# Performance work log

Hardware: AMD Instinct MI355X
Metric: run time of the kernel (lower is better)

The kernel has to match this reference:

```python
import jax, jax.numpy as jnp
import numpy as np

BATCH, SEQ, IN_DIM, HID = 256, 256, 128, 512
KMAX, MID, NCLS = 4, 256, 16  # maxout features, maxout/dense/highway width, output classes


def hard_sigmoid(x):
    return jnp.clip(0.2 * x + 0.5, 0.0, 1.0)


def setup_inputs() -> dict:
    key = jax.random.key(0)
    ks = jax.random.split(key, 20)
    s = 0.05
    d = {
        'x': jax.random.normal(ks[0], (BATCH, SEQ, IN_DIM), jnp.float32),
        'W_z': jax.random.normal(ks[1], (IN_DIM, HID), jnp.float32) * s,
        'W_r': jax.random.normal(ks[2], (IN_DIM, HID), jnp.float32) * s,
        'W_h': jax.random.normal(ks[3], (IN_DIM, HID), jnp.float32) * s,
        'U_z': jax.random.normal(ks[4], (HID, HID), jnp.float32) * s,
        'U_r': jax.random.normal(ks[5], (HID, HID), jnp.float32) * s,
        'U_h': jax.random.normal(ks[6], (HID, HID), jnp.float32) * s,
        'b_z': jax.random.normal(ks[7], (HID,), jnp.float32) * s,
        'b_r': jax.random.normal(ks[8], (HID,), jnp.float32) * s,
        'b_h': jax.random.normal(ks[9], (HID,), jnp.float32) * s,
        'mo_W': jax.random.normal(ks[10], (KMAX, HID, MID), jnp.float32) * s,
        'mo_b': jax.random.normal(ks[11], (KMAX, MID), jnp.float32) * s,
        'd1_W': jax.random.normal(ks[12], (MID, MID), jnp.float32) * s,
        'd1_b': jax.random.normal(ks[13], (MID,), jnp.float32) * s,
        'hw_W': jax.random.normal(ks[14], (MID, MID), jnp.float32) * s,
        'hw_b': jax.random.normal(ks[15], (MID,), jnp.float32) * s,
        'hw_Wc': jax.random.normal(ks[16], (MID, MID), jnp.float32) * s,
        'hw_bc': jax.random.normal(ks[17], (MID,), jnp.float32) * s,
        'd2_W': jax.random.normal(ks[18], (MID, NCLS), jnp.float32) * s,
        'd2_b': jax.random.normal(ks[19], (NCLS,), jnp.float32) * s,
    }
    return d


def reference(x, W_z, W_r, W_h, U_z, U_r, U_h, b_z, b_r, b_h,
              mo_W, mo_b, d1_W, d1_b, hw_W, hw_b, hw_Wc, hw_bc, d2_W, d2_b):
    # ---- Theano-convention GRU (reset applied before U_h matmul) ----
    # Precompute all input projections in one batched GEMM each: [B,S,H]
    xz = jnp.einsum('bsi,ih->bsh', x, W_z) + b_z
    xr = jnp.einsum('bsi,ih->bsh', x, W_r) + b_r
    xh = jnp.einsum('bsi,ih->bsh', x, W_h) + b_h

    def step(h, xs):
        xzt, xrt, xht = xs
        z = hard_sigmoid(xzt + h @ U_z)
        r = hard_sigmoid(xrt + h @ U_r)
        hh = jnp.tanh(xht + (r * h) @ U_h)
        h_new = z * h + (1.0 - z) * hh
        return h_new, None

    h0 = jnp.zeros((x.shape[0], U_z.shape[0]), x.dtype)
    # scan over time axis: move S to leading dim
    xs = (jnp.swapaxes(xz, 0, 1), jnp.swapaxes(xr, 0, 1), jnp.swapaxes(xh, 0, 1))
    h, _ = jax.lax.scan(step, h0, xs)

    # ---- Maxout dense ----
    h = jnp.max(jnp.einsum('bi,kio->bko', h, mo_W) + mo_b, axis=1)
    # ---- Dense (linear) ----
    h = h @ d1_W + d1_b
    # ---- Highway ----
    t = jax.nn.sigmoid(h @ hw_Wc + hw_bc)
    hh = jax.nn.relu(h @ hw_W + hw_b)
    h = t * hh + (1.0 - t) * h
    # ---- Dense + softmax ----
    logits = h @ d2_W + d2_b
    return jax.nn.softmax(logits, axis=-1)
```

## Files before the change

### kernel.cpp

```cpp
#include <hip/hip_runtime.h>
#include <hip/hip_bf16.h>
#include <math.h>

#define BATCH 256
#define SEQN  256
#define INDIM 128
#define HID   512
#define MID   256
#define NCLS  16

#define NG 8
#define RG 32
#define NS 16
#define SC 32

typedef _Float16 half8 __attribute__((ext_vector_type(8)));
typedef float    f32x4 __attribute__((ext_vector_type(4)));

__device__ __forceinline__ half8 cc_load16(const _Float16* p) {
    half8 r;
    asm volatile("global_load_dwordx4 %0, %1, off sc1" : "=&v"(r) : "v"(p));
    return r;
}
__device__ __forceinline__ void cc_wait() {
    asm volatile("s_waitcnt vmcnt(0)" ::: "memory");
    __builtin_amdgcn_sched_barrier(0);
}
__device__ __forceinline__ void cc_store16(_Float16* p, _Float16 v) {
    unsigned short u = __builtin_bit_cast(unsigned short, v);
    asm volatile("global_store_short %0, %1, off sc1" :: "v"(p), "v"(u) : "memory");
}
__device__ __forceinline__ void cc_store_u32(unsigned int* p, unsigned int v) {
    asm volatile("global_store_dword %0, %1, off sc1" :: "v"(p), "v"(v) : "memory");
}
__device__ __forceinline__ unsigned int cc_load_u32(const unsigned int* p) {
    unsigned int r;
    asm volatile("global_load_dword %0, %1, off sc1\n\ts_waitcnt vmcnt(0)"
                 : "=&v"(r) : "v"(p) : "memory");
    return r;
}

__device__ __forceinline__ void wait_flags(const unsigned int* base, int s,
                                           int l, unsigned int tgt) {
    const int slot = l & 15;
    for (;;) {
        unsigned int v = cc_load_u32(base + slot);
        int ok = (slot == s) || (v >= tgt);
        if (__all(ok)) break;
    }
}

__global__ __launch_bounds__(256) void pack_wA(
    const float* __restrict__ Uz, const float* __restrict__ Ur,
    const float* __restrict__ Wz, const float* __restrict__ Wr,
    _Float16* __restrict__ out)
{
    int idx = blockIdx.x * 256 + threadIdx.x;
    int j = idx & 7, l = (idx >> 3) & 63;
    int fr = idx >> 9;
    int kt = fr % 20; int r2 = fr / 20;
    int nt4 = r2 & 3; int s = r2 >> 2;
    int k = kt * 32 + (l >> 4) * 8 + j;
    int col = s * SC + (nt4 & 1) * 16 + (l & 15);
    const float* U = (nt4 < 2) ? Uz : Ur;
    const float* W = (nt4 < 2) ? Wz : Wr;
    float v = (k < HID) ? U[k * HID + col] : W[(k - HID) * HID + col];
    out[idx] = (_Float16)v;
}

__global__ __launch_bounds__(256) void pack_wB(
    const float* __restrict__ Uh, const float* __restrict__ Wh,
    _Float16* __restrict__ out)
{
    int idx = blockIdx.x * 256 + threadIdx.x;
    int j = idx & 7, l = (idx >> 3) & 63;
    int fr = idx >> 9;
    int kt = fr % 20; int r2 = fr / 20;
    int nt2 = r2 & 1; int s = r2 >> 1;
    int k = kt * 32 + (l >> 4) * 8 + j;
    int col = s * SC + nt2 * 16 + (l & 15);
    float v = (k < HID) ? Uh[k * HID + col] : Wh[(k - HID) * HID + col];
    out[idx] = (_Float16)v;
}

__global__ __launch_bounds__(512) void gru_sync(
    const float* __restrict__ x, const _Float16* __restrict__ GWA,
    const _Float16* __restrict__ GWB,
    const float* __restrict__ bz, const float* __restrict__ br,
    const float* __restrict__ bh,
    _Float16* __restrict__ HF, _Float16* __restrict__ VF,
    unsigned int* __restrict__ arr, float* __restrict__ hout)
{
    __shared__ __attribute__((aligned(16))) _Float16 WA[4][20][64][8];
    __shared__ __attribute__((aligned(16))) _Float16 WB[2][20][64][8];
    __shared__ float HO[RG][SC];

    const int tid = threadIdx.x;
    const int w = tid >> 6, l = tid & 63;
    const int bid = blockIdx.x;
    const int g = bid & 7, s = bid >> 3;
    const int m = l & 15;
    const int crow0 = (l >> 4) * 4;

    const int mt  = w & 1;
    const int nt4 = w >> 1;
    const int nt2 = w >> 1;

    {
        const float4* srcA = (const float4*)&GWA[(size_t)s * (4 * 20 * 512)];
        float4* dstA = (float4*)&WA[0][0][0][0];
        for (int i = tid; i < 4 * 20 * 512 / 8; i += 512) dstA[i] = srcA[i];
        const float4* srcB = (const float4*)&GWB[(size_t)s * (2 * 20 * 512)];
        float4* dstB = (float4*)&WB[0][0][0][0];
        for (int i = tid; i < 2 * 20 * 512 / 8; i += 512) dstB[i] = srcB[i];
    }
    for (int i = tid; i < RG * SC; i += 512) ((float*)HO)[i] = 0.f;

    float biasA;
    {
        int col = s * SC + (nt4 & 1) * 16 + m;
        biasA = (nt4 < 2) ? bz[col] : br[col];
    }
    float biasB = 0.f;
    if (w < 4) biasB = bh[s * SC + nt2 * 16 + m];

    unsigned int* f1base = &arr[g * 16];
    unsigned int* f2base = &arr[128 + g * 16];
    unsigned int* f1own  = &arr[g * 16 + s];
    unsigned int* f2own  = &arr[128 + g * 16 + s];
    __syncthreads();

    float zreg[4];
    half8 xfr[4];

    for (int t = 0; t < SEQN; ++t) {
        float4 xa[4], xb[4];
        {
            const float* xp = &x[(((size_t)(g * RG + mt * 16 + m)) * SEQN + t) * INDIM + (l >> 4) * 8];
            #pragma unroll
            for (int kf = 0; kf < 4; ++kf) {
                xa[kf] = *(const float4*)(xp + kf * 32);
                xb[kf] = *(const float4*)(xp + kf * 32 + 4);
            }
        }

        wait_flags(f2base, s, l, (unsigned int)t);

        half8 hfr[16];
        {
            const _Float16* hf = &HF[(size_t)(g * 2 + mt) * 16 * 512];
            #pragma unroll
            for (int kt = 0; kt < 16; ++kt)
                hfr[kt] = cc_load16(hf + kt * 512 + l * 8);
        }
        #pragma unroll
        for (int kf = 0; kf < 4; ++kf) {
            half8 hx;
            hx[0] = (_Float16)xa[kf].x; hx[1] = (_Float16)xa[kf].y;
            hx[2] = (_Float16)xa[kf].z; hx[3] = (_Float16)xa[kf].w;
            hx[4] = (_Float16)xb[kf].x; hx[5] = (_Float16)xb[kf].y;
            hx[6] = (_Float16)xb[kf].z; hx[7] = (_Float16)xb[kf].w;
            xfr[kf] = hx;
        }
        cc_wait();

        {
            f32x4 acc = {0.f, 0.f, 0.f, 0.f};
            #pragma unroll
            for (int kt = 0; kt < 16; ++kt) {
                half8 bf = *(const half8*)&WA[nt4][kt][l][0];
                acc = __builtin_amdgcn_mfma_f32_16x16x32_f16(hfr[kt], bf, acc, 0, 0, 0);
            }
            #pragma unroll
            for (int kf = 0; kf < 4; ++kf) {
                half8 bf = *(const half8*)&WA[nt4][16 + kf][l][0];
                acc = __builtin_amdgcn_mfma_f32_16x16x32_f16(xfr[kf], bf, acc, 0, 0, 0);
            }
            if (nt4 < 2) {
                #pragma unroll
                for (int ri = 0; ri < 4; ++ri) {
                    float pre = acc[ri] + biasA;
                    zreg[ri] = fminf(fmaxf(0.2f * pre + 0.5f, 0.f), 1.f);
                }
            } else {
                #pragma unroll
                for (int ri = 0; ri < 4; ++ri) {
                    float pre = acc[ri] + biasA;
                    float gr = fminf(fmaxf(0.2f * pre + 0.5f, 0.f), 1.f);
                    int rloc = mt * 16 + crow0 + ri;
                    int cs = (nt4 & 1) * 16 + m;
                    float vv = gr * HO[rloc][cs];
                    cc_store16(&VF[(((size_t)(g * 2 + mt) * 16 + s) * 64 +
                                    ((crow0 + ri) + 16 * (cs >> 3))) * 8 + (cs & 7)],
                               (_Float16)vv);
                }
            }
        }

        asm volatile("s_waitcnt vmcnt(0)" ::: "memory");
        __syncthreads();
        if (tid == 0) cc_store_u32(f1own, (unsigned int)(t + 1));

        if (w < 4) {
            wait_flags(f1base, s, l, (unsigned int)(t + 1));

            half8 vfr[16];
            {
                const _Float16* vf = &VF[(size_t)(g * 2 + mt) * 16 * 512];
                #pragma unroll
                for (int kt = 0; kt < 16; ++kt)
                    vfr[kt] = cc_load16(vf + kt * 512 + l * 8);
            }
            cc_wait();

            f32x4 acc2 = {0.f, 0.f, 0.f, 0.f};
            #pragma unroll
            for (int kt = 0; kt < 16; ++kt) {
                half8 bf = *(const half8*)&WB[nt2][kt][l][0];
                acc2 = __builtin_amdgcn_mfma_f32_16x16x32_f16(vfr[kt], bf, acc2, 0, 0, 0);
            }
            #pragma unroll
            for (int kf = 0; kf < 4; ++kf) {
                half8 bf = *(const half8*)&WB[nt2][16 + kf][l][0];
                acc2 = __builtin_amdgcn_mfma_f32_16x16x32_f16(xfr[kf], bf, acc2, 0, 0, 0);
            }
            #pragma unroll
            for (int ri = 0; ri < 4; ++ri) {
                float pre = acc2[ri] + biasB;
                float e  = __expf(2.f * pre);
                float hh = 1.f - 2.f / (e + 1.f);
                int rloc = mt * 16 + crow0 + ri;
                int cs = nt2 * 16 + m;
                float zz = zreg[ri];
                float ho = HO[rloc][cs];
                float hn = zz * ho + (1.f - zz) * hh;
                HO[rloc][cs] = hn;
                cc_store16(&HF[(((size_t)(g * 2 + mt) * 16 + s) * 64 +
                                ((crow0 + ri) + 16 * (cs >> 3))) * 8 + (cs & 7)],
                           (_Float16)hn);
            }
        }

        asm volatile("s_waitcnt vmcnt(0)" ::: "memory");
        __syncthreads();
        if (tid == 0) cc_store_u32(f2own, (unsigned int)(t + 1));
    }

    for (int i = tid; i < RG * SC; i += 512) {
        int r = i >> 5, c = i & 31;
        hout[(size_t)(g * RG + r) * HID + s * SC + c] = HO[r][c];
    }
}

__global__ __launch_bounds__(256) void maxout_k(
    const float* __restrict__ h, const float* __restrict__ moW,
    const float* __restrict__ mob, float* __restrict__ m)
{
    const int ot = blockIdx.x, bt = blockIdx.y;
    __shared__ float sA[32][33];
    __shared__ float sB[4][32][33];
    const int tid = threadIdx.x;
    const int tx = tid & 15, ty = tid >> 4;
    const int b0 = bt * 32, o0 = ot * 32;
    const int lr = tid >> 3, lk4 = (tid & 7) << 2;

    float acc[4][2][2];
    #pragma unroll
    for (int p = 0; p < 4; ++p)
        acc[p][0][0] = acc[p][0][1] = acc[p][1][0] = acc[p][1][1] = 0.f;

    for (int kt = 0; kt < 16; ++kt) {
        const int k0 = kt * 32;
        float4 a = *reinterpret_cast<const float4*>(&h[(b0 + lr) * HID + k0 + lk4]);
        float4 wv[4];
        #pragma unroll
        for (int p = 0; p < 4; ++p)
            wv[p] = *reinterpret_cast<const float4*>(&moW[((size_t)p * HID + k0 + lr) * MID + o0 + lk4]);
        __syncthreads();
        sA[lk4+0][lr] = a.x; sA[lk4+1][lr] = a.y; sA[lk4+2][lr] = a.z; sA[lk4+3][lr] = a.w;
        #pragma unroll
        for (int p = 0; p < 4; ++p) {
            sB[p][lr][lk4+0] = wv[p].x; sB[p][lr][lk4+1] = wv[p].y;
            sB[p][lr][lk4+2] = wv[p].z; sB[p][lr][lk4+3] = wv[p].w;
        }
        __syncthreads();
        #pragma unroll
        for (int kk = 0; kk < 32; ++kk) {
            float a0 = sA[kk][ty*2], a1 = sA[kk][ty*2+1];
            #pragma unroll
            for (int p = 0; p < 4; ++p) {
                float w0 = sB[p][kk][tx*2], w1 = sB[p][kk][tx*2+1];
                acc[p][0][0] += a0*w0; acc[p][0][1] += a0*w1;
                acc[p][1][0] += a1*w0; acc[p][1][1] += a1*w1;
            }
        }
    }

    #pragma unroll
    for (int q = 0; q < 2; ++q)
        #pragma unroll
        for (int c = 0; c < 2; ++c) {
            const int row = b0 + ty*2 + q, col = o0 + tx*2 + c;
            float best = -1e30f;
            #pragma unroll
            for (int p = 0; p < 4; ++p)
                best = fmaxf(best, acc[p][q][c] + mob[p * MID + col]);
            m[row * MID + col] = best;
        }
}

__global__ __launch_bounds__(256) void dense1_k(
    const float* __restrict__ m, const float* __restrict__ W,
    const float* __restrict__ b, float* __restrict__ a1)
{
    const int jt = blockIdx.x, bt = blockIdx.y;
    __shared__ float sA[32][33];
    __shared__ float sB[32][33];
    const int tid = threadIdx.x;
    const int tx = tid & 15, ty = tid >> 4;
    const int b0 = bt * 32, j0 = jt * 32;
    const int lr = tid >> 3, lk4 = (tid & 7) << 2;

    float acc[2][2] = {{0.f,0.f},{0.f,0.f}};

    for (int kt = 0; kt < 8; ++kt) {
        const int k0 = kt * 32;
        float4 a  = *reinterpret_cast<const float4*>(&m[(b0 + lr) * MID + k0 + lk4]);
        float4 bv = *reinterpret_cast<const float4*>(&W[(k0 + lr) * MID + j0 + lk4]);
        __syncthreads();
        sA[lk4+0][lr] = a.x; sA[lk4+1][lr] = a.y; sA[lk4+2][lr] = a.z; sA[lk4+3][lr] = a.w;
        sB[lr][lk4+0] = bv.x; sB[lr][lk4+1] = bv.y; sB[lr][lk4+2] = bv.z; sB[lr][lk4+3] = bv.w;
        __syncthreads();
        #pragma unroll
        for (int kk = 0; kk < 32; ++kk) {
            float a0 = sA[kk][ty*2], a1v = sA[kk][ty*2+1];
            float w0 = sB[kk][tx*2], w1 = sB[kk][tx*2+1];
            acc[0][0] += a0*w0; acc[0][1] += a0*w1;
            acc[1][0] += a1v*w0; acc[1][1] += a1v*w1;
        }
    }

    #pragma unroll
    for (int q = 0; q < 2; ++q)
        #pragma unroll
        for (int c = 0; c < 2; ++c) {
            const int row = b0 + ty*2 + q, col = j0 + tx*2 + c;
            a1[row * MID + col] = acc[q][c] + b[col];
        }
}

__global__ __launch_bounds__(256) void highway_k(
    const float* __restrict__ a1,
    const float* __restrict__ hwW, const float* __restrict__ hwb,
    const float* __restrict__ hwWc, const float* __restrict__ hwbc,
    float* __restrict__ h2)
{
    const int jt = blockIdx.x, bt = blockIdx.y;
    __shared__ float sA[32][33];
    __shared__ float sBh[32][33];
    __shared__ float sBc[32][33];
    const int tid = threadIdx.x;
    const int tx = tid & 15, ty = tid >> 4;
    const int b0 = bt * 32, j0 = jt * 32;
    const int lr = tid >> 3, lk4 = (tid & 7) << 2;

    float acch[2][2] = {{0.f,0.f},{0.f,0.f}};
    float accc[2][2] = {{0.f,0.f},{0.f,0.f}};

    for (int kt = 0; kt < 8; ++kt) {
        const int k0 = kt * 32;
        float4 a   = *reinterpret_cast<const float4*>(&a1[(b0 + lr) * MID + k0 + lk4]);
        float4 bh4 = *reinterpret_cast<const float4*>(&hwW[(k0 + lr) * MID + j0 + lk4]);
        float4 bc4 = *reinterpret_cast<const float4*>(&hwWc[(k0 + lr) * MID + j0 + lk4]);
        __syncthreads();
        sA[lk4+0][lr] = a.x; sA[lk4+1][lr] = a.y; sA[lk4+2][lr] = a.z; sA[lk4+3][lr] = a.w;
        sBh[lr][lk4+0] = bh4.x; sBh[lr][lk4+1] = bh4.y; sBh[lr][lk4+2] = bh4.z; sBh[lr][lk4+3] = bh4.w;
        sBc[lr][lk4+0] = bc4.x; sBc[lr][lk4+1] = bc4.y; sBc[lr][lk4+2] = bc4.z; sBc[lr][lk4+3] = bc4.w;
        __syncthreads();
        #pragma unroll
        for (int kk = 0; kk < 32; ++kk) {
            float a0 = sA[kk][ty*2], a1v = sA[kk][ty*2+1];
            float h0 = sBh[kk][tx*2], h1 = sBh[kk][tx*2+1];
            float c0 = sBc[kk][tx*2], c1 = sBc[kk][tx*2+1];
            acch[0][0] += a0*h0; acch[0][1] += a0*h1;
            acch[1][0] += a1v*h0; acch[1][1] += a1v*h1;
            accc[0][0] += a0*c0; accc[0][1] += a0*c1;
            accc[1][0] += a1v*c0; accc[1][1] += a1v*c1;
        }
    }

    #pragma unroll
    for (int q = 0; q < 2; ++q)
        #pragma unroll
        for (int c = 0; c < 2; ++c) {
            const int row = b0 + ty*2 + q, col = j0 + tx*2 + c;
            float tt = 1.f / (1.f + expf(-(accc[q][c] + hwbc[col])));
            float hp = fmaxf(acch[q][c] + hwb[col], 0.f);
            float av = a1[row * MID + col];
            h2[row * MID + col] = tt * hp + (1.f - tt) * av;
        }
}

__global__ __launch_bounds__(256) void d2_softmax(
    const float* __restrict__ h2, const float* __restrict__ W,
    const float* __restrict__ b, float* __restrict__ out)
{
    const int b0 = blockIdx.x * 16;
    const int r = threadIdx.x >> 4, c = threadIdx.x & 15;
    const int row = b0 + r;

    float acc = b[c];
    for (int i = 0; i < MID; ++i)
        acc += h2[row * MID + i] * W[i * NCLS + c];

    float mx = acc;
    #pragma unroll
    for (int off = 8; off; off >>= 1)
        mx = fmaxf(mx, __shfl_xor(mx, off, 16));
    float e = expf(acc - mx);
    float sm = e;
    #pragma unroll
    for (int off = 8; off; off >>= 1)
        sm += __shfl_xor(sm, off, 16);
    out[row * NCLS + c] = e / sm;
}

extern "C" void kernel_launch(void* const* d_in, const int* in_sizes, int n_in,
                              void* d_out, int out_size, void* d_ws, size_t ws_size,
                              hipStream_t stream) {
    (void)in_sizes; (void)n_in; (void)out_size; (void)ws_size;

    const float* x    = (const float*)d_in[0];
    const float* Wz   = (const float*)d_in[1];
    const float* Wr   = (const float*)d_in[2];
    const float* Wh   = (const float*)d_in[3];
    const float* Uz   = (const float*)d_in[4];
    const float* Ur   = (const float*)d_in[5];
    const float* Uh   = (const float*)d_in[6];
    const float* bz   = (const float*)d_in[7];
    const float* br   = (const float*)d_in[8];
    const float* bh   = (const float*)d_in[9];
    const float* moW  = (const float*)d_in[10];
    const float* mob  = (const float*)d_in[11];
    const float* d1W  = (const float*)d_in[12];
    const float* d1b  = (const float*)d_in[13];
    const float* hwW  = (const float*)d_in[14];
    const float* hwb  = (const float*)d_in[15];
    const float* hwWc = (const float*)d_in[16];
    const float* hwbc = (const float*)d_in[17];
    const float* d2W  = (const float*)d_in[18];
    const float* d2b  = (const float*)d_in[19];
    float* out = (float*)d_out;

    char* ws = (char*)d_ws;
    _Float16* GWA = (_Float16*)(ws + 0);
    _Float16* GWB = (_Float16*)(ws + 1310720);
    _Float16* HF  = (_Float16*)(ws + 1966080);
    _Float16* VF  = (_Float16*)(ws + 2228224);
    unsigned int* arr = (unsigned int*)(ws + 2490368);
    float*    hbuf = (float*)(ws + 2494464);
    float*    mxb = (float*)(ws + 0);
    float*    a1b = (float*)(ws + 262144);
    float*    h2b = (float*)(ws + 524288);

    hipMemsetAsync(HF, 0, 262144, stream);
    hipMemsetAsync(arr, 0, 4096, stream);

    pack_wA<<<2560, 256, 0, stream>>>(Uz, Ur, Wz, Wr, GWA);
    pack_wB<<<1280, 256, 0, stream>>>(Uh, Wh, GWB);

    gru_sync<<<128, 512, 0, stream>>>(x, GWA, GWB, bz, br, bh, HF, VF, arr, hbuf);

    dim3 blk(256);
    maxout_k<<<dim3(8, 8), blk, 0, stream>>>(hbuf, moW, mob, mxb);
    dense1_k<<<dim3(8, 8), blk, 0, stream>>>(mxb, d1W, d1b, a1b);
    highway_k<<<dim3(8, 8), blk, 0, stream>>>(a1b, hwW, hwb, hwWc, hwbc, h2b);
    d2_softmax<<<16, blk, 0, stream>>>(h2b, d2W, d2b, out);
}
```

Before: 1.742 ms.

## Replace block-wide barriers with per-wave flag handshakes and double-buffer hidden state

Splits the GRU block's waves into r-gate producers and z/candidate consumers that synchronize through per-wave global flags instead of __syncthreads plus one block flag. The shared hidden-state buffer is double-buffered by timestep parity, so the next step's writes do not race with readers of the current step. The aim is to cut the barrier and serialization latency on the recurrent critical path. In exchange there are many more flag slots to poll, with finer-grained spinning and a larger workspace layout.

```diff
diff --git a/kernel.cpp b/kernel.cpp
--- a/kernel.cpp
+++ b/kernel.cpp
@@ -40,13 +40,12 @@
     return r;
 }
 
-__device__ __forceinline__ void wait_flags(const unsigned int* base, int s,
+__device__ __forceinline__ void wait_slots(const unsigned int* base, int mt,
                                            int l, unsigned int tgt) {
-    const int slot = l & 15;
+    const int slot = ((l & 15) << 2) + (((l >> 4) & 1) << 1) + mt;
     for (;;) {
         unsigned int v = cc_load_u32(base + slot);
-        int ok = (slot == s) || (v >= tgt);
-        if (__all(ok)) break;
+        if (__all((int)(v >= tgt))) break;
     }
 }
 
@@ -102,10 +101,6 @@
     const int m = l & 15;
     const int crow0 = (l >> 4) * 4;
 
-    const int mt  = w & 1;
-    const int nt4 = w >> 1;
-    const int nt2 = w >> 1;
-
     {
         const float4* srcA = (const float4*)&GWA[(size_t)s * (4 * 20 * 512)];
         float4* dstA = (float4*)&WA[0][0][0][0];
@@ -116,136 +111,169 @@
     }
     for (int i = tid; i < RG * SC; i += 512) ((float*)HO)[i] = 0.f;
 
-    float biasA;
-    {
-        int col = s * SC + (nt4 & 1) * 16 + m;
-        biasA = (nt4 < 2) ? bz[col] : br[col];
-    }
-    float biasB = 0.f;
-    if (w < 4) biasB = bh[s * SC + nt2 * 16 + m];
-
-    unsigned int* f1base = &arr[g * 16];
-    unsigned int* f2base = &arr[128 + g * 16];
-    unsigned int* f1own  = &arr[g * 16 + s];
-    unsigned int* f2own  = &arr[128 + g * 16 + s];
+    unsigned int* vfl = &arr[g * 64];
+    unsigned int* hfl = &arr[512 + g * 64];
+    const size_t HFBUF = (size_t)NG * 2 * 16 * 512;
+
     __syncthreads();
 
-    float zreg[4];
-    half8 xfr[4];
-
-    for (int t = 0; t < SEQN; ++t) {
-        float4 xa[4], xb[4];
-        {
+    if (w >= 4) {
+        const int mt = w & 1;
+        const int ct = (w - 4) >> 1;
+        const float biasA = br[s * SC + ct * 16 + m];
+        unsigned int* myflag = &vfl[s * 4 + (w - 4)];
+
+        for (int t = 0; t < SEQN; ++t) {
             const float* xp = &x[(((size_t)(g * RG + mt * 16 + m)) * SEQN + t) * INDIM + (l >> 4) * 8];
+            float4 xa[4], xb[4];
             #pragma unroll
             for (int kf = 0; kf < 4; ++kf) {
                 xa[kf] = *(const float4*)(xp + kf * 32);
                 xb[kf] = *(const float4*)(xp + kf * 32 + 4);
             }
-        }
-
-        wait_flags(f2base, s, l, (unsigned int)t);
-
-        half8 hfr[16];
-        {
-            const _Float16* hf = &HF[(size_t)(g * 2 + mt) * 16 * 512];
+
+            wait_slots(hfl, mt, l, (unsigned int)t);
+
+            half8 hfr[16];
+            const _Float16* hf = &HF[(t & 1) * HFBUF + (size_t)(g * 2 + mt) * 16 * 512];
             #pragma unroll
             for (int kt = 0; kt < 16; ++kt)
                 hfr[kt] = cc_load16(hf + kt * 512 + l * 8);
-        }
-        #pragma unroll
-        for (int kf = 0; kf < 4; ++kf) {
-            half8 hx;
-            hx[0] = (_Float16)xa[kf].x; hx[1] = (_Float16)xa[kf].y;
-            hx[2] = (_Float16)xa[kf].z; hx[3] = (_Float16)xa[kf].w;
-            hx[4] = (_Float16)xb[kf].x; hx[5] = (_Float16)xb[kf].y;
-            hx[6] = (_Float16)xb[kf].z; hx[7] = (_Float16)xb[kf].w;
-            xfr[kf] = hx;
-        }
-        cc_wait();
-
-        {
+
+            half8 xfr[4];
+            #pragma unroll
+            for (int kf = 0; kf < 4; ++kf) {
+                half8 hx;
+                hx[0] = (_Float16)xa[kf].x; hx[1] = (_Float16)xa[kf].y;
+                hx[2] = (_Float16)xa[kf].z; hx[3] = (_Float16)xa[kf].w;
+                hx[4] = (_Float16)xb[kf].x; hx[5] = (_Float16)xb[kf].y;
+                hx[6] = (_Float16)xb[kf].z; hx[7] = (_Float16)xb[kf].w;
+                xfr[kf] = hx;
+            }
+            cc_wait();
+
             f32x4 acc = {0.f, 0.f, 0.f, 0.f};
             #pragma unroll
             for (int kt = 0; kt < 16; ++kt) {
-                half8 bf = *(const half8*)&WA[nt4][kt][l][0];
+                half8 bf = *(const half8*)&WA[2 + ct][kt][l][0];
                 acc = __builtin_amdgcn_mfma_f32_16x16x32_f16(hfr[kt], bf, acc, 0, 0, 0);
             }
             #pragma unroll
             for (int kf = 0; kf < 4; ++kf) {
-                half8 bf = *(const half8*)&WA[nt4][16 + kf][l][0];
+                half8 bf = *(const half8*)&WA[2 + ct][16 + kf][l][0];
                 acc = __builtin_amdgcn_mfma_f32_16x16x32_f16(xfr[kf], bf, acc, 0, 0, 0);
             }
-            if (nt4 < 2) {
-                #pragma unroll
-                for (int ri = 0; ri < 4; ++ri) {
-                    float pre = acc[ri] + biasA;
-                    zreg[ri] = fminf(fmaxf(0.2f * pre + 0.5f, 0.f), 1.f);
-                }
-            } else {
-                #pragma unroll
-                for (int ri = 0; ri < 4; ++ri) {
-                    float pre = acc[ri] + biasA;
-                    float gr = fminf(fmaxf(0.2f * pre + 0.5f, 0.f), 1.f);
-                    int rloc = mt * 16 + crow0 + ri;
-                    int cs = (nt4 & 1) * 16 + m;
-                    float vv = gr * HO[rloc][cs];
-                    cc_store16(&VF[(((size_t)(g * 2 + mt) * 16 + s) * 64 +
-                                    ((crow0 + ri) + 16 * (cs >> 3))) * 8 + (cs & 7)],
-                               (_Float16)vv);
-                }
-            }
-        }
-
-        asm volatile("s_waitcnt vmcnt(0)" ::: "memory");
-        __syncthreads();
-        if (tid == 0) cc_store_u32(f1own, (unsigned int)(t + 1));
-
-        if (w < 4) {
-            wait_flags(f1base, s, l, (unsigned int)(t + 1));
+            #pragma unroll
+            for (int ri = 0; ri < 4; ++ri) {
+                float pre = acc[ri] + biasA;
+                float gr = fminf(fmaxf(0.2f * pre + 0.5f, 0.f), 1.f);
+                int rloc = mt * 16 + crow0 + ri;
+                int cs = ct * 16 + m;
+                float vv = gr * HO[rloc][cs];
+                cc_store16(&VF[(((size_t)(g * 2 + mt) * 16 + s) * 64 +
+                                ((crow0 + ri) + 16 * (cs >> 3))) * 8 + (cs & 7)],
+                           (_Float16)vv);
+            }
+            asm volatile("s_waitcnt vmcnt(0)" ::: "memory");
+            if (l == 0) cc_store_u32(myflag, (unsigned int)(t + 1));
+        }
+    } else {
+        const int mt = w & 1;
+        const int ct = w >> 1;
+        const float biasA = bz[s * SC + ct * 16 + m];
+        const float biasB = bh[s * SC + ct * 16 + m];
+        unsigned int* myflag = &hfl[s * 4 + w];
+
+        for (int t = 0; t < SEQN; ++t) {
+            const float* xp = &x[(((size_t)(g * RG + mt * 16 + m)) * SEQN + t) * INDIM + (l >> 4) * 8];
+            float4 xa[4], xb[4];
+            #pragma unroll
+            for (int kf = 0; kf < 4; ++kf) {
+                xa[kf] = *(const float4*)(xp + kf * 32);
+                xb[kf] = *(const float4*)(xp + kf * 32 + 4);
+            }
+
+            wait_slots(hfl, mt, l, (unsigned int)t);
+
+            half8 hfr[16];
+            const _Float16* hf = &HF[(t & 1) * HFBUF + (size_t)(g * 2 + mt) * 16 * 512];
+            #pragma unroll
+            for (int kt = 0; kt < 16; ++kt)
+                hfr[kt] = cc_load16(hf + kt * 512 + l * 8);
+
+            half8 xfr[4];
+            #pragma unroll
+            for (int kf = 0; kf < 4; ++kf) {
+                half8 hx;
+                hx[0] = (_Float16)xa[kf].x; hx[1] = (_Float16)xa[kf].y;
+                hx[2] = (_Float16)xa[kf].z; hx[3] = (_Float16)xa[kf].w;
+                hx[4] = (_Float16)xb[kf].x; hx[5] = (_Float16)xb[kf].y;
+                hx[6] = (_Float16)xb[kf].z; hx[7] = (_Float16)xb[kf].w;
+                xfr[kf] = hx;
+            }
+            cc_wait();
+
+            f32x4 acc = {0.f, 0.f, 0.f, 0.f};
+            #pragma unroll
+            for (int kt = 0; kt < 16; ++kt) {
+                half8 bf = *(const half8*)&WA[ct][kt][l][0];
+                acc = __builtin_amdgcn_mfma_f32_16x16x32_f16(hfr[kt], bf, acc, 0, 0, 0);
+            }
+            #pragma unroll
+            for (int kf = 0; kf < 4; ++kf) {
+                half8 bf = *(const half8*)&WA[ct][16 + kf][l][0];
+                acc = __builtin_amdgcn_mfma_f32_16x16x32_f16(xfr[kf], bf, acc, 0, 0, 0);
+            }
+            float zreg[4];
+            #pragma unroll
+            for (int ri = 0; ri < 4; ++ri) {
+                float pre = acc[ri] + biasA;
+                zreg[ri] = fminf(fmaxf(0.2f * pre + 0.5f, 0.f), 1.f);
+            }
+
+            wait_slots(vfl, mt, l, (unsigned int)(t + 1));
 
             half8 vfr[16];
-            {
-                const _Float16* vf = &VF[(size_t)(g * 2 + mt) * 16 * 512];
-                #pragma unroll
-                for (int kt = 0; kt < 16; ++kt)
-                    vfr[kt] = cc_load16(vf + kt * 512 + l * 8);
-            }
+            const _Float16* vf = &VF[(size_t)(g * 2 + mt) * 16 * 512];
+            #pragma unroll
+            for (int kt = 0; kt < 16; ++kt)
+                vfr[kt] = cc_load16(vf + kt * 512 + l * 8);
             cc_wait();
 
             f32x4 acc2 = {0.f, 0.f, 0.f, 0.f};
             #pragma unroll
             for (int kt = 0; kt < 16; ++kt) {
-                half8 bf = *(const half8*)&WB[nt2][kt][l][0];
+                half8 bf = *(const half8*)&WB[ct][kt][l][0];
                 acc2 = __builtin_amdgcn_mfma_f32_16x16x32_f16(vfr[kt], bf, acc2, 0, 0, 0);
             }
             #pragma unroll
             for (int kf = 0; kf < 4; ++kf) {
-                half8 bf = *(const half8*)&WB[nt2][16 + kf][l][0];
+                half8 bf = *(const half8*)&WB[ct][16 + kf][l][0];
                 acc2 = __builtin_amdgcn_mfma_f32_16x16x32_f16(xfr[kf], bf, acc2, 0, 0, 0);
             }
+
+            _Float16* hfo = &HF[((t + 1) & 1) * HFBUF];
             #pragma unroll
             for (int ri = 0; ri < 4; ++ri) {
                 float pre = acc2[ri] + biasB;
                 float e  = __expf(2.f * pre);
                 float hh = 1.f - 2.f / (e + 1.f);
                 int rloc = mt * 16 + crow0 + ri;
-                int cs = nt2 * 16 + m;
+                int cs = ct * 16 + m;
                 float zz = zreg[ri];
                 float ho = HO[rloc][cs];
                 float hn = zz * ho + (1.f - zz) * hh;
                 HO[rloc][cs] = hn;
-                cc_store16(&HF[(((size_t)(g * 2 + mt) * 16 + s) * 64 +
-                                ((crow0 + ri) + 16 * (cs >> 3))) * 8 + (cs & 7)],
+                cc_store16(&hfo[(((size_t)(g * 2 + mt) * 16 + s) * 64 +
+                                 ((crow0 + ri) + 16 * (cs >> 3))) * 8 + (cs & 7)],
                            (_Float16)hn);
             }
-        }
-
-        asm volatile("s_waitcnt vmcnt(0)" ::: "memory");
-        __syncthreads();
-        if (tid == 0) cc_store_u32(f2own, (unsigned int)(t + 1));
-    }
-
+            asm volatile("s_waitcnt vmcnt(0) lgkmcnt(0)" ::: "memory");
+            if (l == 0) cc_store_u32(myflag, (unsigned int)(t + 1));
+        }
+    }
+
+    __syncthreads();
     for (int i = tid; i < RG * SC; i += 512) {
         int r = i >> 5, c = i & 31;
         hout[(size_t)(g * RG + r) * HID + s * SC + c] = HO[r][c];
@@ -456,14 +484,14 @@
     _Float16* GWA = (_Float16*)(ws + 0);
     _Float16* GWB = (_Float16*)(ws + 1310720);
     _Float16* HF  = (_Float16*)(ws + 1966080);
-    _Float16* VF  = (_Float16*)(ws + 2228224);
-    unsigned int* arr = (unsigned int*)(ws + 2490368);
-    float*    hbuf = (float*)(ws + 2494464);
+    _Float16* VF  = (_Float16*)(ws + 2490368);
+    unsigned int* arr = (unsigned int*)(ws + 2752512);
+    float*    hbuf = (float*)(ws + 2756608);
     float*    mxb = (float*)(ws + 0);
     float*    a1b = (float*)(ws + 262144);
     float*    h2b = (float*)(ws + 524288);
 
-    hipMemsetAsync(HF, 0, 262144, stream);
+    hipMemsetAsync(HF, 0, 524288, stream);
     hipMemsetAsync(arr, 0, 4096, stream);
 
     pack_wA<<<2560, 256, 0, stream>>>(Uz, Ur, Wz, Wr, GWA);
```

After: 5.677 ms. 3.26x slower.
